# Kernel tuning notes

Hardware: AMD Instinct MI355X
Metric: run time of the kernel (lower is better)

The kernel has to match this reference:

```python
import jax, jax.numpy as jnp
import numpy as np

B, D, C, H = 65536, 256, 128, 1024
SPLIT = D // 2           # transformed half (odd indices under 'even' mask)
NET_IN = (D - SPLIT) + C # unchanged half + cond


def setup_inputs() -> dict:
    key = jax.random.key(0)
    ks = jax.random.split(key, 10)
    s = 0.02
    return {
        "x": jax.random.normal(ks[0], (B, D), jnp.float32),
        "cond": jax.random.normal(ks[1], (B, C), jnp.float32),
        "W1": jax.random.normal(ks[2], (NET_IN, H), jnp.float32) * s,
        "b1": jnp.zeros((H,), jnp.float32),
        "W2": jax.random.normal(ks[3], (H, H), jnp.float32) * s,
        "b2": jnp.zeros((H,), jnp.float32),
        "Ws": jax.random.normal(ks[4], (H, SPLIT), jnp.float32) * s,
        "bs": jnp.zeros((SPLIT,), jnp.float32),
        "Wt": jax.random.normal(ks[5], (H, SPLIT), jnp.float32) * s,
        "bt": jnp.zeros((SPLIT,), jnp.float32),
    }


def reference(x, cond, W1, b1, W2, b2, Ws, bs, Wt, bt):
    d = x.shape[1]
    even = jnp.arange(0, d, 2)  # mask==1 -> unchanged (x1)
    odd = jnp.arange(1, d, 2)   # mask==0 -> transformed (x2)
    x1u = x[:, even]            # (B, d - d//2)
    x2u = x[:, odd]             # (B, d//2)
    h = jax.nn.relu(jnp.concatenate([x1u, cond], axis=1) @ W1 + b1)
    h = jax.nn.relu(h @ W2 + b2)
    log_s = jnp.tanh(h @ Ws + bs)
    t = h @ Wt + bt
    x2t = x2u * jnp.exp(log_s) + t
    out = jnp.zeros_like(x).at[:, even].set(x1u).at[:, odd].set(x2t)
    log_det = jnp.sum(log_s, axis=1)
    return out, log_det
```

## Files before the change

### kernel.cpp

```cpp
#include <hip/hip_runtime.h>
#include <hip/hip_bf16.h>
#include <math.h>

#define B_ROWS 65536
#define D_DIM 256
#define C_DIM 128
#define H_DIM 1024

typedef __bf16 bf16x8 __attribute__((ext_vector_type(8)));
typedef float f32x4 __attribute__((ext_vector_type(4)));
typedef short short8 __attribute__((ext_vector_type(8)));

__device__ __forceinline__ unsigned short f2bf(float f) {
    unsigned int u = __float_as_uint(f);
    u += 0x7fffu + ((u >> 16) & 1u);
    return (unsigned short)(u >> 16);
}

__device__ __forceinline__ void gl2lds16(const void* g, void* l) {
    __builtin_amdgcn_global_load_lds(
        (const __attribute__((address_space(1))) unsigned int*)g,
        (__attribute__((address_space(3))) unsigned int*)l, 16, 0, 0);
}

__device__ __forceinline__ bf16x8 ds_read_b128_asm(const short* p) {
    bf16x8 r;
    asm volatile("ds_read_b128 %0, %1"
                 : "=v"(r)
                 : "v"((const __attribute__((address_space(3))) short*)p));
    return r;
}

__device__ __forceinline__ void swizzle_mn(int id, int mtiles, int& m, int& n) {
    if ((mtiles & 7) == 0) {
        int g = id >> 6, r = id & 63;
        m = g * 8 + (r & 7);
        n = r >> 3;
    } else {
        m = id >> 3;
        n = id & 7;
    }
}

__global__ void transpose_bf16(const float* __restrict__ src, short* __restrict__ dst,
                               int R, int C, int total) {
    int tid = blockIdx.x * 256 + threadIdx.x;
    if (tid >= total) return;
    int per = R >> 3;
    int n = tid / per;
    int k0 = (tid - n * per) << 3;
    short8 o;
#pragma unroll
    for (int j = 0; j < 8; ++j) o[j] = (short)f2bf(src[(size_t)(k0 + j) * C + n]);
    *(short8*)&dst[(size_t)n * R + k0] = o;
}

__global__ void prep_b3(const float* __restrict__ bs, const float* __restrict__ bt,
                        float* __restrict__ b3) {
    int i = threadIdx.x;
    b3[i] = (i < 128) ? bs[i] : bt[i - 128];
}

__global__ __launch_bounds__(256) void prep_a(
    const float* __restrict__ x, const float* __restrict__ cond,
    short* __restrict__ A) {
    int t = blockIdx.x * 256 + threadIdx.x;
    int m = t >> 5, seg = t & 31;
    short8 o;
    if (seg < 16) {
        const float4* p = (const float4*)(x + (size_t)m * 256 + seg * 16);
        float4 a = p[0], b = p[1], c = p[2], d = p[3];
        o[0] = (short)f2bf(a.x); o[1] = (short)f2bf(a.z);
        o[2] = (short)f2bf(b.x); o[3] = (short)f2bf(b.z);
        o[4] = (short)f2bf(c.x); o[5] = (short)f2bf(c.z);
        o[6] = (short)f2bf(d.x); o[7] = (short)f2bf(d.z);
    } else {
        const float4* p = (const float4*)(cond + (size_t)m * 128 + (seg - 16) * 8);
        float4 a = p[0], b = p[1];
        o[0] = (short)f2bf(a.x); o[1] = (short)f2bf(a.y);
        o[2] = (short)f2bf(a.z); o[3] = (short)f2bf(a.w);
        o[4] = (short)f2bf(b.x); o[5] = (short)f2bf(b.y);
        o[6] = (short)f2bf(b.z); o[7] = (short)f2bf(b.w);
    }
    *(short8*)&A[(size_t)m * 256 + seg * 8] = o;
}

__global__ __launch_bounds__(256) void gemm_tn(
    const short* __restrict__ A, const short* __restrict__ Bw,
    const float* __restrict__ bias, unsigned short* __restrict__ Cout,
    int mtiles, int N, int K) {
    constexpr int BK = 64;
    __shared__ __align__(16) short As[128 * BK];
    __shared__ __align__(16) short Bs[128 * BK];
    const int tid = threadIdx.x;
    const int lane = tid & 63;
    const int wave = tid >> 6;
    int mt, nt;
    swizzle_mn(blockIdx.x, mtiles, mt, nt);
    const int tm = mt * 128, tn = nt * 128;
    const int mo = (wave >> 1) * 64;
    const int no = (wave & 1) * 64;

    f32x4 acc[4][4];
#pragma unroll
    for (int i = 0; i < 4; ++i)
#pragma unroll
        for (int j = 0; j < 4; ++j) acc[i][j] = f32x4{0.f, 0.f, 0.f, 0.f};

    const int srow = lane >> 3;
    const int skb = (lane & 7) ^ srow;

    for (int kc = 0; kc < K; kc += BK) {
        __syncthreads();
#pragma unroll
        for (int i = 0; i < 4; ++i) {
            int c = wave * 4 + i;
            int row = c * 8 + srow;
            gl2lds16(A + (size_t)(tm + row) * K + kc + skb * 8, &As[c * 512]);
            gl2lds16(Bw + (size_t)(tn + row) * K + kc + skb * 8, &Bs[c * 512]);
        }
        __syncthreads();
#pragma unroll
        for (int kk = 0; kk < 2; ++kk) {
            bf16x8 af[4], bfr[4];
            int kb = kk * 4 + (lane >> 4);
#pragma unroll
            for (int t = 0; t < 4; ++t) {
                int r = mo + t * 16 + (lane & 15);
                af[t] = *(const bf16x8*)&As[r * BK + ((kb ^ (r & 7)) << 3)];
                int n = no + t * 16 + (lane & 15);
                bfr[t] = *(const bf16x8*)&Bs[n * BK + ((kb ^ (n & 7)) << 3)];
            }
#pragma unroll
            for (int i = 0; i < 4; ++i)
#pragma unroll
                for (int j = 0; j < 4; ++j)
                    acc[i][j] = __builtin_amdgcn_mfma_f32_16x16x32_bf16(
                        af[i], bfr[j], acc[i][j], 0, 0, 0);
        }
    }

#pragma unroll
    for (int j = 0; j < 4; ++j) {
        int col = tn + no + j * 16 + (lane & 15);
        float bb = bias[col];
#pragma unroll
        for (int i = 0; i < 4; ++i) {
            int row0 = tm + mo + i * 16 + ((lane >> 4) << 2);
            f32x4 v = acc[i][j];
#pragma unroll
            for (int rr = 0; rr < 4; ++rr)
                Cout[(size_t)(row0 + rr) * N + col] = f2bf(fmaxf(v[rr] + bb, 0.f));
        }
    }
}

template<int K>
__global__ __launch_bounds__(512, 2) void gemm2_8ph(
    const short* __restrict__ A, const short* __restrict__ Bw,
    const float* __restrict__ bias, unsigned short* __restrict__ Cout) {
    constexpr int NT = K / 64;
    constexpr unsigned OFF_A0 = 0, OFF_B0 = 16384, OFF_A1 = 32768, OFF_B1 = 49152;
    __shared__ __align__(16) short smem[65536];

    const int tid = threadIdx.x;
    const int lane = tid & 63;
    const int wave = tid >> 6;
    const int wm = wave >> 2;
    const int wn = wave & 3;
    const int l15 = lane & 15;
    const int quad = lane >> 4;
    const int srow = lane >> 3;
    const int skb8 = ((lane & 7) ^ srow) << 3;

    const int id = blockIdx.x, nwg = gridDim.x;
    const int xcd = id & 7, lid = id >> 3;
    const int q = nwg >> 3, r = nwg & 7;
    const int wgid = (xcd < r ? xcd * (q + 1) : r * (q + 1) + (xcd - r) * q) + lid;
    const int mt = wgid >> 2, nt = wgid & 3;
    const size_t Abase = (size_t)(mt * 256) * K;
    const size_t Bbase = (size_t)(nt * 256) * K;

    f32x4 acc[8][4];
#pragma unroll
    for (int m = 0; m < 8; ++m)
#pragma unroll
        for (int n = 0; n < 4; ++n) acc[m][n] = f32x4{0.f, 0.f, 0.f, 0.f};

    auto stage2 = [&](unsigned off, const short* g, size_t rowbase, int kc, int c0, int c1) {
        gl2lds16(g + rowbase + (size_t)(c0 * 8 + srow) * K + kc + skb8, smem + off + c0 * 512);
        gl2lds16(g + rowbase + (size_t)(c1 * 8 + srow) * K + kc + skb8, smem + off + c1 * 512);
    };
    auto stageU = [&](int u, unsigned aOff, unsigned bOff, int kc) {
        if (u == 0)      stage2(bOff, Bw, Bbase, kc, wave * 2, wave * 2 + 1);
        else if (u == 1) stage2(bOff, Bw, Bbase, kc, 16 + wave * 2, 17 + wave * 2);
        else if (u == 2) stage2(aOff, A, Abase, kc, wave, 16 + wave);
        else             stage2(aOff, A, Abase, kc, 8 + wave, 24 + wave);
    };

    const unsigned x0 = (unsigned)((quad ^ (l15 & 7)) << 3);
    const unsigned x1 = (unsigned)(((4 + quad) ^ (l15 & 7)) << 3);

    auto window = [&](int w, unsigned caOff, unsigned cbOff, unsigned naOff, unsigned nbOff) {
        const int kc1 = (w + 1) << 6, kc2 = (w + 2) << 6;
        const short* aA = smem + caOff + ((wm << 7) + l15) * 64;
        const short* aB = smem + cbOff + ((wn << 6) + l15) * 64;
        bf16x8 bfr[4][2], af[2][2];

#pragma unroll
        for (int n = 0; n < 4; ++n) {
            bfr[n][0] = ds_read_b128_asm(aB + n * 1024 + x0);
            bfr[n][1] = ds_read_b128_asm(aB + n * 1024 + x1);
        }
#pragma unroll
        for (int mm = 0; mm < 2; ++mm) {
            af[mm][0] = ds_read_b128_asm(aA + mm * 1024 + x0);
            af[mm][1] = ds_read_b128_asm(aA + mm * 1024 + x1);
        }
        if (w + 1 < NT) stageU(3, naOff, nbOff, kc1);
        __builtin_amdgcn_sched_barrier(0);
        __builtin_amdgcn_s_barrier();
        asm volatile("s_waitcnt lgkmcnt(0)" ::: "memory");
        __builtin_amdgcn_sched_barrier(0);
        __builtin_amdgcn_s_setprio(1);
#pragma unroll
        for (int kk = 0; kk < 2; ++kk)
#pragma unroll
            for (int mm = 0; mm < 2; ++mm)
#pragma unroll
                for (int n = 0; n < 4; ++n)
                    acc[mm][n] = __builtin_amdgcn_mfma_f32_16x16x32_bf16(
                        af[mm][kk], bfr[n][kk], acc[mm][n], 0, 0, 0);
        __builtin_amdgcn_s_setprio(0);

#pragma unroll
        for (int ph = 1; ph < 4; ++ph) {
#pragma unroll
            for (int mm = 0; mm < 2; ++mm) {
                af[mm][0] = ds_read_b128_asm(aA + (ph * 2 + mm) * 1024 + x0);
                af[mm][1] = ds_read_b128_asm(aA + (ph * 2 + mm) * 1024 + x1);
            }
            if (w + 2 < NT) stageU(ph - 1, caOff, cbOff, kc2);
            if (ph == 3) {
                if (w < NT - 2)
                    asm volatile("s_waitcnt vmcnt(6)" ::: "memory");
                else
                    asm volatile("s_waitcnt vmcnt(0)" ::: "memory");
            }
            __builtin_amdgcn_sched_barrier(0);
            __builtin_amdgcn_s_barrier();
            asm volatile("s_waitcnt lgkmcnt(0)" ::: "memory");
            __builtin_amdgcn_sched_barrier(0);
            __builtin_amdgcn_s_setprio(1);
#pragma unroll
            for (int kk = 0; kk < 2; ++kk)
#pragma unroll
                for (int mm = 0; mm < 2; ++mm)
#pragma unroll
                    for (int n = 0; n < 4; ++n)
                        acc[ph * 2 + mm][n] = __builtin_amdgcn_mfma_f32_16x16x32_bf16(
                            af[mm][kk], bfr[n][kk], acc[ph * 2 + mm][n], 0, 0, 0);
            __builtin_amdgcn_s_setprio(0);
        }
    };

    stageU(0, OFF_A0, OFF_B0, 0);
    stageU(1, OFF_A0, OFF_B0, 0);
    stageU(2, OFF_A0, OFF_B0, 0);
    stageU(3, OFF_A0, OFF_B0, 0);
    stageU(0, OFF_A1, OFF_B1, 64);
    stageU(1, OFF_A1, OFF_B1, 64);
    stageU(2, OFF_A1, OFF_B1, 64);
    asm volatile("s_waitcnt vmcnt(6)" ::: "memory");
    __builtin_amdgcn_sched_barrier(0);
    __builtin_amdgcn_s_barrier();

#pragma unroll 1
    for (int w = 0; w < NT; w += 2) {
        window(w, OFF_A0, OFF_B0, OFF_A1, OFF_B1);
        window(w + 1, OFF_A1, OFF_B1, OFF_A0, OFF_B0);
    }

    __syncthreads();
    unsigned short* cs = (unsigned short*)smem;
#pragma unroll
    for (int n = 0; n < 4; ++n) {
        int colblk = wn * 4 + n;
        int col = (colblk << 4) + l15;
        float bb = bias[nt * 256 + col];
#pragma unroll
        for (int m = 0; m < 8; ++m) {
            int row = (wm << 7) + m * 16 + (quad << 2);
#pragma unroll
            for (int rr = 0; rr < 4; ++rr) {
                int rw = row + rr;
                int sb = colblk ^ ((rw >> 2) & 3);
                cs[rw * 256 + (sb << 4) + l15] = f2bf(fmaxf(acc[m][n][rr] + bb, 0.f));
            }
        }
    }
    __syncthreads();
    const size_t cbase = (size_t)(mt * 256) * 1024 + nt * 256;
    const int rloc = tid >> 5, cchunk = tid & 31;
#pragma unroll
    for (int rnd = 0; rnd < 16; ++rnd) {
        int rw = rnd * 16 + rloc;
        int blk = cchunk >> 1, half = cchunk & 1;
        int sb = blk ^ ((rw >> 2) & 3);
        short8 v = *(const short8*)&cs[rw * 256 + (sb << 4) + half * 8];
        *(short8*)((unsigned short*)Cout + cbase + (size_t)rw * 1024 + cchunk * 8) = v;
    }
}

__global__ __launch_bounds__(256) void gemm3_final(
    const short* __restrict__ H2, const short* __restrict__ W3T,
    const float* __restrict__ b3, const float* __restrict__ x,
    float* __restrict__ out, float* __restrict__ logdet) {
    constexpr int BK = 64, K = 1024;
    __shared__ __align__(16) char raw[40960];
    __shared__ float rowsum[64];
    short* As = (short*)raw;
    short* Bs = (short*)(raw + 8192);
    float* Tbuf = (float*)raw;
    const int tid = threadIdx.x;
    const int lane = tid & 63;
    const int wave = tid >> 6;
    const int tm = blockIdx.x * 64;
    const int srow = lane >> 3;
    const int skb = (lane & 7) ^ srow;
    const int l15 = lane & 15;
    const int quad = lane >> 4;

    if (tid < 64) rowsum[tid] = 0.f;

    f32x4 acc[4][4];
#pragma unroll
    for (int i = 0; i < 4; ++i)
#pragma unroll
        for (int j = 0; j < 4; ++j) acc[i][j] = f32x4{0.f, 0.f, 0.f, 0.f};

    for (int kc = 0; kc < K; kc += BK) {
        __syncthreads();
#pragma unroll
        for (int i = 0; i < 10; ++i) {
            int c = wave * 10 + i;
            if (c < 8) {
                int row = c * 8 + srow;
                gl2lds16(H2 + (size_t)(tm + row) * K + kc + skb * 8, &As[c * 512]);
            } else {
                int row = (c - 8) * 8 + srow;
                gl2lds16(W3T + (size_t)row * K + kc + skb * 8, &Bs[(c - 8) * 512]);
            }
        }
        __syncthreads();
#pragma unroll
        for (int kk = 0; kk < 2; ++kk) {
            int kb = kk * 4 + quad;
            bf16x8 af[4], bfr[4];
#pragma unroll
            for (int mt = 0; mt < 4; ++mt) {
                int r = mt * 16 + l15;
                af[mt] = *(const bf16x8*)&As[r * BK + ((kb ^ (r & 7)) << 3)];
            }
#pragma unroll
            for (int nt = 0; nt < 4; ++nt) {
                int n = wave * 64 + nt * 16 + l15;
                bfr[nt] = *(const bf16x8*)&Bs[n * BK + ((kb ^ (n & 7)) << 3)];
            }
#pragma unroll
            for (int mt = 0; mt < 4; ++mt)
#pragma unroll
                for (int nt = 0; nt < 4; ++nt)
                    acc[mt][nt] = __builtin_amdgcn_mfma_f32_16x16x32_bf16(
                        af[mt], bfr[nt], acc[mt][nt], 0, 0, 0);
        }
    }

    __syncthreads();
    if (wave >= 2) {
#pragma unroll
        for (int nt = 0; nt < 4; ++nt) {
            int col = wave * 64 + nt * 16 + l15;
            float bb = b3[col];
            int cl = col - 128;
#pragma unroll
            for (int mt = 0; mt < 4; ++mt) {
#pragma unroll
                for (int rr = 0; rr < 4; ++rr) {
                    int m = mt * 16 + quad * 4 + rr;
                    Tbuf[m * 132 + cl] = acc[mt][nt][rr] + bb;
                }
            }
        }
    }
    __syncthreads();
    if (wave < 2) {
#pragma unroll
        for (int mt = 0; mt < 4; ++mt) {
#pragma unroll
            for (int rr = 0; rr < 4; ++rr) {
                int m = mt * 16 + quad * 4 + rr;
                int grow = tm + m;
                float s = 0.f;
#pragma unroll
                for (int nt = 0; nt < 4; ++nt) {
                    int j = wave * 64 + nt * 16 + l15;
                    float p = acc[mt][nt][rr] + b3[j];
                    p = fminf(fmaxf(p, -15.f), 15.f);
                    float e2 = __expf(2.f * p);
                    float ls = (e2 - 1.f) / (e2 + 1.f);
                    s += ls;
                    float tt = Tbuf[m * 132 + j];
                    float2 xv = *(const float2*)&x[(size_t)grow * 256 + 2 * j];
                    float2 ov;
                    ov.x = xv.x;
                    ov.y = xv.y * __expf(ls) + tt;
                    *(float2*)&out[(size_t)grow * 256 + 2 * j] = ov;
                }
                s += __shfl_xor(s, 1);
                s += __shfl_xor(s, 2);
                s += __shfl_xor(s, 4);
                s += __shfl_xor(s, 8);
                if (l15 == 0) atomicAdd(&rowsum[m], s);
            }
        }
    }
    __syncthreads();
    if (tid < 64) logdet[tm + tid] = rowsum[tid];
}

extern "C" void kernel_launch(void* const* d_in, const int* in_sizes, int n_in,
                              void* d_out, int out_size, void* d_ws, size_t ws_size,
                              hipStream_t stream) {
    const float* x = (const float*)d_in[0];
    const float* cond = (const float*)d_in[1];
    const float* W1 = (const float*)d_in[2];
    const float* b1 = (const float*)d_in[3];
    const float* W2 = (const float*)d_in[4];
    const float* b2 = (const float*)d_in[5];
    const float* Wsp = (const float*)d_in[6];
    const float* bs = (const float*)d_in[7];
    const float* Wtp = (const float*)d_in[8];
    const float* bt = (const float*)d_in[9];

    char* ws = (char*)d_ws;
    short* W1T = (short*)(ws);
    short* W2T = (short*)(ws + 524288ull);
    short* W3T = (short*)(ws + 2621440ull);
    float* b3  = (float*)(ws + 3145728ull);
    short* Aprep = (short*)(ws + 3149824ull);
    const size_t chunk_base = 3149824ull + 33554432ull;

    int n_chunks = 1;
    while (n_chunks < 512) {
        size_t rp = (size_t)B_ROWS / n_chunks;
        if (chunk_base + rp * 4096ull <= ws_size) break;
        n_chunks *= 2;
    }
    const size_t RP = (size_t)B_ROWS / n_chunks;

    float* out = (float*)d_out;
    float* logdet = out + (size_t)B_ROWS * D_DIM;

    transpose_bf16<<<(32768 + 255) / 256, 256, 0, stream>>>(W1, W1T, 256, 1024, 32768);
    transpose_bf16<<<(131072 + 255) / 256, 256, 0, stream>>>(W2, W2T, 1024, 1024, 131072);
    transpose_bf16<<<(16384 + 255) / 256, 256, 0, stream>>>(Wsp, W3T, 1024, 128, 16384);
    transpose_bf16<<<(16384 + 255) / 256, 256, 0, stream>>>(Wtp, W3T + 131072, 1024, 128, 16384);
    prep_b3<<<1, 256, 0, stream>>>(bs, bt, b3);
    prep_a<<<B_ROWS * 32 / 256, 256, 0, stream>>>(x, cond, Aprep);

    for (int c = 0; c < n_chunks; ++c) {
        const size_t r0 = (size_t)c * RP;
        short* H1 = (short*)(ws + chunk_base);
        short* H2 = (short*)(ws + chunk_base + 2048ull * RP);
        const int mtiles = (int)(RP / 128);

        if ((RP & 255) == 0) {
            gemm2_8ph<256><<<(int)(RP / 256) * 4, 512, 0, stream>>>(
                Aprep + r0 * 256, W1T, b1, (unsigned short*)H1);
            gemm2_8ph<1024><<<(int)(RP / 256) * 4, 512, 0, stream>>>(
                H1, W2T, b2, (unsigned short*)H2);
        } else {
            gemm_tn<<<mtiles * 8, 256, 0, stream>>>(
                Aprep + r0 * 256, W1T, b1, (unsigned short*)H1, mtiles, H_DIM, 256);
            gemm_tn<<<mtiles * 8, 256, 0, stream>>>(
                H1, W2T, b2, (unsigned short*)H2, mtiles, H_DIM, H_DIM);
        }
        gemm3_final<<<(int)(RP / 64), 256, 0, stream>>>(
            H2, W3T, b3, x + r0 * D_DIM, out + r0 * D_DIM, logdet + r0);
    }
}
```

Before: 460.1 us.

## Software-pipeline LDS fragment reads one phase ahead of MFMA issue

Restructures the GEMM main loop into per-phase slots, where each slot runs the MFMAs for the previous phase's fragments and then issues the LDS reads for the current phase. The LDS read latency can then overlap with matrix-core work instead of sitting behind an lgkmcnt wait right before the MFMAs. Fragment registers move out of the window lambda so they stay live across slots, and a tail MFMA batch drains the last phase. This raises register pressure and makes the barrier and waitcnt ordering more delicate, since global-to-LDS staging is now issued after the barrier in each slot.

```diff
diff --git a/kernel.cpp b/kernel.cpp
--- a/kernel.cpp
+++ b/kernel.cpp
@@ -187,6 +187,9 @@
 #pragma unroll
         for (int n = 0; n < 4; ++n) acc[m][n] = f32x4{0.f, 0.f, 0.f, 0.f};
 
+    bf16x8 af[2][2] = {};
+    bf16x8 bfr[4][2] = {};
+
     auto stage2 = [&](unsigned off, const short* g, size_t rowbase, int kc, int c0, int c1) {
         gl2lds16(g + rowbase + (size_t)(c0 * 8 + srow) * K + kc + skb8, smem + off + c0 * 512);
         gl2lds16(g + rowbase + (size_t)(c1 * 8 + srow) * K + kc + skb8, smem + off + c1 * 512);
@@ -201,67 +204,50 @@
     const unsigned x0 = (unsigned)((quad ^ (l15 & 7)) << 3);
     const unsigned x1 = (unsigned)(((4 + quad) ^ (l15 & 7)) << 3);
 
-    auto window = [&](int w, unsigned caOff, unsigned cbOff, unsigned naOff, unsigned nbOff) {
-        const int kc1 = (w + 1) << 6, kc2 = (w + 2) << 6;
+    auto mfma8 = [&](int pprev) {
+        __builtin_amdgcn_s_setprio(1);
+#pragma unroll
+        for (int kk = 0; kk < 2; ++kk)
+#pragma unroll
+            for (int mm = 0; mm < 2; ++mm)
+#pragma unroll
+                for (int n = 0; n < 4; ++n)
+                    acc[pprev * 2 + mm][n] = __builtin_amdgcn_mfma_f32_16x16x32_bf16(
+                        af[mm][kk], bfr[n][kk], acc[pprev * 2 + mm][n], 0, 0, 0);
+        __builtin_amdgcn_s_setprio(0);
+    };
+
+    auto slot = [&](int ph, int w, unsigned caOff, unsigned cbOff,
+                    unsigned naOff, unsigned nbOff) {
+        if (ph & 1) {
+            if (w < NT - 2) asm volatile("s_waitcnt vmcnt(6)" ::: "memory");
+            else            asm volatile("s_waitcnt vmcnt(0)" ::: "memory");
+        }
+        __builtin_amdgcn_sched_barrier(0);
+        __builtin_amdgcn_s_barrier();
+        __builtin_amdgcn_sched_barrier(0);
+        if (ph == 0) { if (w + 1 < NT) stageU(3, naOff, nbOff, (w + 1) << 6); }
+        else         { if (w + 2 < NT) stageU(ph - 1, caOff, cbOff, (w + 2) << 6); }
+        __builtin_amdgcn_sched_barrier(0);
+        asm volatile("s_waitcnt lgkmcnt(0)" ::: "memory");
+        __builtin_amdgcn_sched_barrier(0);
+        mfma8((ph + 3) & 3);
+        __builtin_amdgcn_sched_barrier(0);
         const short* aA = smem + caOff + ((wm << 7) + l15) * 64;
         const short* aB = smem + cbOff + ((wn << 6) + l15) * 64;
-        bf16x8 bfr[4][2], af[2][2];
-
-#pragma unroll
-        for (int n = 0; n < 4; ++n) {
-            bfr[n][0] = ds_read_b128_asm(aB + n * 1024 + x0);
-            bfr[n][1] = ds_read_b128_asm(aB + n * 1024 + x1);
+        if (ph == 0) {
+#pragma unroll
+            for (int n = 0; n < 4; ++n) {
+                bfr[n][0] = ds_read_b128_asm(aB + n * 1024 + x0);
+                bfr[n][1] = ds_read_b128_asm(aB + n * 1024 + x1);
+            }
         }
 #pragma unroll
         for (int mm = 0; mm < 2; ++mm) {
-            af[mm][0] = ds_read_b128_asm(aA + mm * 1024 + x0);
-            af[mm][1] = ds_read_b128_asm(aA + mm * 1024 + x1);
-        }
-        if (w + 1 < NT) stageU(3, naOff, nbOff, kc1);
-        __builtin_amdgcn_sched_barrier(0);
-        __builtin_amdgcn_s_barrier();
-        asm volatile("s_waitcnt lgkmcnt(0)" ::: "memory");
-        __builtin_amdgcn_sched_barrier(0);
-        __builtin_amdgcn_s_setprio(1);
-#pragma unroll
-        for (int kk = 0; kk < 2; ++kk)
-#pragma unroll
-            for (int mm = 0; mm < 2; ++mm)
-#pragma unroll
-                for (int n = 0; n < 4; ++n)
-                    acc[mm][n] = __builtin_amdgcn_mfma_f32_16x16x32_bf16(
-                        af[mm][kk], bfr[n][kk], acc[mm][n], 0, 0, 0);
-        __builtin_amdgcn_s_setprio(0);
-
-#pragma unroll
-        for (int ph = 1; ph < 4; ++ph) {
-#pragma unroll
-            for (int mm = 0; mm < 2; ++mm) {
-                af[mm][0] = ds_read_b128_asm(aA + (ph * 2 + mm) * 1024 + x0);
-                af[mm][1] = ds_read_b128_asm(aA + (ph * 2 + mm) * 1024 + x1);
-            }
-            if (w + 2 < NT) stageU(ph - 1, caOff, cbOff, kc2);
-            if (ph == 3) {
-                if (w < NT - 2)
-                    asm volatile("s_waitcnt vmcnt(6)" ::: "memory");
-                else
-                    asm volatile("s_waitcnt vmcnt(0)" ::: "memory");
-            }
-            __builtin_amdgcn_sched_barrier(0);
-            __builtin_amdgcn_s_barrier();
-            asm volatile("s_waitcnt lgkmcnt(0)" ::: "memory");
-            __builtin_amdgcn_sched_barrier(0);
-            __builtin_amdgcn_s_setprio(1);
-#pragma unroll
-            for (int kk = 0; kk < 2; ++kk)
-#pragma unroll
-                for (int mm = 0; mm < 2; ++mm)
-#pragma unroll
-                    for (int n = 0; n < 4; ++n)
-                        acc[ph * 2 + mm][n] = __builtin_amdgcn_mfma_f32_16x16x32_bf16(
-                            af[mm][kk], bfr[n][kk], acc[ph * 2 + mm][n], 0, 0, 0);
-            __builtin_amdgcn_s_setprio(0);
-        }
+            af[mm][0] = ds_read_b128_asm(aA + (ph * 2 + mm) * 1024 + x0);
+            af[mm][1] = ds_read_b128_asm(aA + (ph * 2 + mm) * 1024 + x1);
+        }
+        __builtin_amdgcn_sched_barrier(0);
     };
 
     stageU(0, OFF_A0, OFF_B0, 0);
@@ -272,14 +258,19 @@
     stageU(1, OFF_A1, OFF_B1, 64);
     stageU(2, OFF_A1, OFF_B1, 64);
     asm volatile("s_waitcnt vmcnt(6)" ::: "memory");
-    __builtin_amdgcn_sched_barrier(0);
-    __builtin_amdgcn_s_barrier();
 
 #pragma unroll 1
     for (int w = 0; w < NT; w += 2) {
-        window(w, OFF_A0, OFF_B0, OFF_A1, OFF_B1);
-        window(w + 1, OFF_A1, OFF_B1, OFF_A0, OFF_B0);
-    }
+#pragma unroll
+        for (int ph = 0; ph < 4; ++ph)
+            slot(ph, w, OFF_A0, OFF_B0, OFF_A1, OFF_B1);
+#pragma unroll
+        for (int ph = 0; ph < 4; ++ph)
+            slot(ph, w + 1, OFF_A1, OFF_B1, OFF_A0, OFF_B0);
+    }
+    asm volatile("s_waitcnt lgkmcnt(0)" ::: "memory");
+    __builtin_amdgcn_sched_barrier(0);
+    mfma8(3);
 
     __syncthreads();
     unsigned short* cs = (unsigned short*)smem;
```

Measured after the change: 458.6 us. Within noise of the previous version (-0.3%).
